# Optimization experiments

Hardware: AMD Instinct MI355X
Metric: run time of the kernel (lower is better)

## Reference

```python
import jax, jax.numpy as jnp
import numpy as np

# Static multi-level feature-map geometry (h, w) per level.
SPATIAL_SHAPES = np.array([[92, 92], [46, 46], [23, 23], [12, 12]], dtype=np.int32)
_AREAS = SPATIAL_SHAPES[:, 0] * SPATIAL_SHAPES[:, 1]
LEVEL_START = np.concatenate([[0], np.cumsum(_AREAS)[:-1]]).astype(np.int32)
LEN_IN = int(_AREAS.sum())  # 11253
N_HEADS, N_LEVELS, N_POINTS = 8, 4, 4
D_MODEL, D_HEAD = 256, 64


def setup_inputs() -> dict:
    key = jax.random.key(0)
    ks = jax.random.split(key, 12)
    N, Lq = 4, 1000
    s = 0.02
    f32 = jnp.float32
    return {
        'query': jax.random.normal(ks[0], (N, Lq, D_MODEL), f32),
        'reference_points': jax.random.uniform(ks[1], (N, Lq, N_LEVELS, 2), f32),
        'input_flatten': jax.random.normal(ks[2], (N, LEN_IN, D_MODEL), f32),
        'input_spatial_shapes': jnp.asarray(SPATIAL_SHAPES),
        'input_level_start_index': jnp.asarray(LEVEL_START),
        'W_off': jax.random.normal(ks[3], (N_HEADS * N_LEVELS * N_POINTS * 2, D_MODEL), f32) * s,
        'b_off': jax.random.normal(ks[4], (N_HEADS * N_LEVELS * N_POINTS * 2,), f32) * 0.5,
        'W_attn': jax.random.normal(ks[5], (N_HEADS * N_LEVELS * N_POINTS, D_MODEL), f32) * s,
        'b_attn': jax.random.normal(ks[6], (N_HEADS * N_LEVELS * N_POINTS,), f32) * s,
        'W_val': jax.random.normal(ks[7], (N_HEADS * D_HEAD, D_MODEL), f32) * s,
        'b_val': jnp.zeros((N_HEADS * D_HEAD,), f32),
        'W_out': jax.random.normal(ks[8], (D_MODEL, N_HEADS * D_HEAD), f32) * s,
        'b_out': jnp.zeros((D_MODEL,), f32),
    }


def _ms_deform_attn(value, sampling_locations, attention_weights):
    # value: [N, Len_in, H, D]; locations: [N, Lq, H, L, P, 2] in [0,1];
    # weights: [N, Lq, H, L, P] -> out [N, Lq, H*D]
    N, _, H, D = value.shape
    Lq, L, P = sampling_locations.shape[1], sampling_locations.shape[3], sampling_locations.shape[4]
    out = jnp.zeros((N, H, Lq, D), value.dtype)
    for l in range(L):
        h, w = int(SPATIAL_SHAPES[l, 0]), int(SPATIAL_SHAPES[l, 1])
        st = int(LEVEL_START[l])
        # per-level value as [N*H, h*w, D]
        v = value[:, st:st + h * w].transpose(0, 2, 1, 3).reshape(N * H, h * w, D)
        loc = sampling_locations[:, :, :, l].transpose(0, 2, 1, 3, 4).reshape(N * H, Lq * P, 2)
        aw = attention_weights[:, :, :, l].transpose(0, 2, 1, 3).reshape(N * H, Lq * P)
        # grid_sample align_corners=False convention (matches CUDA kernel)
        x = loc[..., 0] * w - 0.5
        y = loc[..., 1] * h - 0.5
        x0 = jnp.floor(x)
        y0 = jnp.floor(y)
        lx, ly = x - x0, y - y0
        x0i = x0.astype(jnp.int32)
        y0i = y0.astype(jnp.int32)

        def gather(yi, xi):
            valid = ((xi >= 0) & (xi < w) & (yi >= 0) & (yi < h)).astype(v.dtype)
            idx = jnp.clip(yi, 0, h - 1) * w + jnp.clip(xi, 0, w - 1)
            g = jnp.take_along_axis(v, idx[..., None], axis=1)  # [N*H, Lq*P, D]
            return g * valid[..., None]

        sampled = (gather(y0i, x0i) * ((1 - lx) * (1 - ly))[..., None]
                   + gather(y0i, x0i + 1) * (lx * (1 - ly))[..., None]
                   + gather(y0i + 1, x0i) * ((1 - lx) * ly)[..., None]
                   + gather(y0i + 1, x0i + 1) * (lx * ly)[..., None])
        out = out + (sampled * aw[..., None]).reshape(N, H, Lq, P, D).sum(axis=3)
    return out.transpose(0, 2, 1, 3).reshape(N, Lq, H * D)


def reference(query, reference_points, input_flatten, input_spatial_shapes,
              input_level_start_index, W_off, b_off, W_attn, b_attn,
              W_val, b_val, W_out, b_out):
    N, Lq, _ = query.shape
    Lin = input_flatten.shape[1]
    H, L, P, D = N_HEADS, N_LEVELS, N_POINTS, D_HEAD
    value = (input_flatten @ W_val.T + b_val).reshape(N, Lin, H, D)
    off = (query @ W_off.T + b_off).reshape(N, Lq, H, L, P, 2)
    aw = jax.nn.softmax((query @ W_attn.T + b_attn).reshape(N, Lq, H, L * P), axis=-1)
    aw = aw.reshape(N, Lq, H, L, P)
    # offset normalizer is (w, h) per level
    norm = jnp.asarray(SPATIAL_SHAPES[:, ::-1].copy(), jnp.float32)  # [L, 2]
    loc = reference_points[:, :, None, :, None, :] + off / norm[None, None, None, :, None, :]
    out = _ms_deform_attn(value, loc, aw)
    return out @ W_out.T + b_out
```

## Files before the change

### kernel.cpp

```cpp
#include <hip/hip_runtime.h>


typedef __attribute__((ext_vector_type(4))) float f32x4;
typedef __attribute__((ext_vector_type(8))) short bf16x8;
typedef __attribute__((ext_vector_type(4))) short bf16x4;

static __device__ __forceinline__ unsigned short f2bf(float f) {
    unsigned u = __builtin_bit_cast(unsigned, f);
    u += 0x7FFFu + ((u >> 16) & 1u);
    return (unsigned short)(u >> 16);
}
static __device__ __forceinline__ float bflo(unsigned d) {
    return __builtin_bit_cast(float, d << 16);
}
static __device__ __forceinline__ float bfhi(unsigned d) {
    return __builtin_bit_cast(float, d & 0xffff0000u);
}
static __device__ __forceinline__ void gload_lds16(const void* g, void* l) {
    __builtin_amdgcn_global_load_lds(
        (const __attribute__((address_space(1))) void*)g,
        (__attribute__((address_space(3))) void*)l, 16, 0, 0);
}

__global__ __launch_bounds__(256)
void cvt_k(const float* __restrict__ s0, const float* __restrict__ s1,
           const float* __restrict__ s2, const float* __restrict__ s3,
           const float* __restrict__ s4, const float* __restrict__ s5,
           unsigned short* __restrict__ dst) {
    const size_t i8 = ((size_t)blockIdx.x * 256 + threadIdx.x) * 8;
    if (i8 >= 12907520u) return;
    const float* sp; size_t loc;
    if (i8 < 11523072u)      { sp = s0; loc = i8; }
    else if (i8 < 12547072u) { sp = s1; loc = i8 - 11523072u; }
    else if (i8 < 12612608u) { sp = s2; loc = i8 - 12547072u; }
    else if (i8 < 12645376u) { sp = s3; loc = i8 - 12612608u; }
    else if (i8 < 12776448u) { sp = s4; loc = i8 - 12645376u; }
    else                     { sp = s5; loc = i8 - 12776448u; }
    f32x4 a = *(const f32x4*)(sp + loc);
    f32x4 b = *(const f32x4*)(sp + loc + 4);
    bf16x8 r;
    r[0] = f2bf(a[0]); r[1] = f2bf(a[1]); r[2] = f2bf(a[2]); r[3] = f2bf(a[3]);
    r[4] = f2bf(b[0]); r[5] = f2bf(b[1]); r[6] = f2bf(b[2]); r[7] = f2bf(b[3]);
    *(bf16x8*)(dst + i8) = r;
}

template<int MODE>
__global__ __launch_bounds__(256)
void gemm_bf16_tn(const unsigned short* __restrict__ A,
                  const unsigned short* __restrict__ B,
                  const float* __restrict__ bias, const float* __restrict__ bias2,
                  void* __restrict__ Cv, int M, int N, int K) {
    __shared__ __align__(16) char smem[65536];

    const int tid = threadIdx.x, lane = tid & 63, w = tid >> 6;
    const int wm = w >> 1, wn = w & 1;
    int bm, bn;
    if (MODE == 1) {
        const int bid = blockIdx.x;
        const int xcd = bid & 7;
        const int j   = bid >> 3;
        bm = xcd * 44 + (j >> 2);
        bn = j & 3;
    } else {
        bm = blockIdx.x; bn = blockIdx.y;
    }

    const int r8 = lane >> 3;
    const int colsrc = (((lane & 7) ^ r8) << 4);
    const char* pa[4]; const char* pb[4];
#pragma unroll
    for (int j = 0; j < 4; j++) {
        int ra = bm * 128 + j * 32 + w * 8 + r8; ra = ra < M ? ra : M - 1;
        int rb = bn * 128 + j * 32 + w * 8 + r8; rb = rb < N ? rb : N - 1;
        pa[j] = (const char*)A + (size_t)ra * ((size_t)K * 2) + colsrc;
        pb[j] = (const char*)B + (size_t)rb * ((size_t)K * 2) + colsrc;
    }
    const int ldso = w << 10;
    const int NT = K >> 6;

    f32x4 acc[4][4] = {};
    const int fr = lane & 15, fq = lane >> 4;
    const int k8b = fq << 4;
    const int swzR = (fr & 7) << 4;

#pragma unroll
    for (int j = 0; j < 4; j++) {
        gload_lds16(pa[j], smem + j * 4096 + ldso);
        gload_lds16(pb[j], smem + 16384 + j * 4096 + ldso);
    }
    __syncthreads();

    for (int t = 0; t < NT; ++t) {
        const int cur = (t & 1) << 15;
        if (t + 1 < NT) {
            const int nxt = ((t + 1) & 1) << 15;
            const int off = (t + 1) << 7;
#pragma unroll
            for (int j = 0; j < 4; j++) {
                gload_lds16(pa[j] + off, smem + nxt + j * 4096 + ldso);
                gload_lds16(pb[j] + off, smem + nxt + 16384 + j * 4096 + ldso);
            }
        }
#pragma unroll
        for (int kk = 0; kk < 2; ++kk) {
            const int ko = ((kk << 6) + k8b) ^ swzR;
            bf16x8 af[4], bv[4];
#pragma unroll
            for (int m = 0; m < 4; m++)
                af[m] = *(const bf16x8*)(smem + cur + ((wm * 64 + m * 16 + fr) << 7) + ko);
#pragma unroll
            for (int nn = 0; nn < 4; nn++)
                bv[nn] = *(const bf16x8*)(smem + cur + 16384 + ((wn * 64 + nn * 16 + fr) << 7) + ko);
#pragma unroll
            for (int m = 0; m < 4; m++)
#pragma unroll
                for (int nn = 0; nn < 4; nn++)
                    acc[m][nn] = __builtin_amdgcn_mfma_f32_16x16x32_bf16(
                        af[m], bv[nn], acc[m][nn], 0, 0, 0);
        }
        __syncthreads();
    }

    if (MODE != 1) {
        float* C = (float*)Cv;
        const int crow0 = bm * 128 + wm * 64 + fq * 4;
        const int ccol0 = bn * 128 + wn * 64 + fr;
#pragma unroll
        for (int m = 0; m < 4; m++) {
#pragma unroll
            for (int nn = 0; nn < 4; nn++) {
                const int col = ccol0 + nn * 16;
                const float bv2 = (MODE == 2 && col >= 256) ? bias2[col - 256]
                                                            : bias[col];
#pragma unroll
                for (int j = 0; j < 4; j++) {
                    const int row = crow0 + m * 16 + j;
                    if (row < M) C[(size_t)row * N + col] = acc[m][nn][j] + bv2;
                }
            }
        }
    } else {
        unsigned short* tile = (unsigned short*)smem + (size_t)w * (64 * 68);
        const int hh = bn * 2 + wn;
        float bvs[4];
#pragma unroll
        for (int nn = 0; nn < 4; nn++) bvs[nn] = bias[hh * 64 + nn * 16 + fr];
#pragma unroll
        for (int m = 0; m < 4; m++)
#pragma unroll
            for (int nn = 0; nn < 4; nn++)
#pragma unroll
                for (int j = 0; j < 4; j++)
                    tile[(m * 16 + fq * 4 + j) * 68 + nn * 16 + fr] =
                        f2bf(acc[m][nn][j] + bvs[nn]);
        __syncthreads();
        unsigned short* VT = (unsigned short*)Cv;
        const int q4 = (lane & 15) * 4;
        const int prow = lane >> 4;
#pragma unroll
        for (int it = 0; it < 16; ++it) {
            const int pl = it * 4 + prow;
            const int pixg = bm * 128 + wm * 64 + pl;
            if (pixg < M) {
                const int n = pixg / 11253;
                const int pix = pixg - n * 11253;
                bf16x4 v = *(const bf16x4*)&tile[pl * 68 + q4];
                *(bf16x4*)(VT + ((size_t)(n * 8 + hh) * 11253 + pix) * 64 + q4) = v;
            }
        }
    }
}

__global__ __launch_bounds__(256)
void sample_k(const unsigned short* __restrict__ valueT,
              const float* __restrict__ refp,
              const float* __restrict__ fused,
              unsigned int* __restrict__ msout)
{
    const int bid = blockIdx.x;
    const int xcd = bid & 7;
    const int jj  = bid >> 3;
    const int sl  = jj / 250;
    const int qb  = jj - sl * 250;
    const int nh  = xcd * 4 + sl;
    const int q   = __builtin_amdgcn_readfirstlane(qb * 4 + (threadIdx.x >> 6));
    const int lane = threadIdx.x & 63;
    const int g    = lane >> 5;
    const int n = nh >> 3, h = nh & 7;
    const int nq = n * 1000 + q;

    const float* lgp = fused + (size_t)nq * 384 + 256 + h * 16;
    float mx = lgp[0];
#pragma unroll
    for (int pp = 1; pp < 16; pp++) mx = fmaxf(mx, lgp[pp]);
    float s = 0.f;
#pragma unroll
    for (int pp = 0; pp < 16; pp++) s += __expf(lgp[pp] - mx);

    const int p  = lane & 15;
    const int lv = p >> 2;
    const int W  = lv == 0 ? 92 : lv == 1 ? 46 : lv == 2 ? 23 : 12;
    const int st = lv == 0 ? 0 : lv == 1 ? 8464 : lv == 2 ? 10580 : 11109;

    const float a  = __expf(lgp[p] - mx) / s;
    const float rx = refp[(size_t)nq * 8 + lv * 2 + 0];
    const float ry = refp[(size_t)nq * 8 + lv * 2 + 1];
    const float ox = fused[(size_t)nq * 384 + h * 32 + p * 2 + 0];
    const float oy = fused[(size_t)nq * 384 + h * 32 + p * 2 + 1];

    const float x = rx * (float)W + ox - 0.5f;
    const float y = ry * (float)W + oy - 0.5f;
    const float xf = floorf(x), yf = floorf(y);
    const int x0 = (int)xf, y0 = (int)yf;
    const float lx = x - xf, ly = y - yf;
    const int xb = min(max(x0, 0), W - 2);
    const int yb = min(max(y0, 0), W - 2);
    const float wx0 = (xb     == x0) ? (1.f - lx) : ((xb     == x0 + 1) ? lx : 0.f);
    const float wx1 = (xb + 1 == x0) ? (1.f - lx) : ((xb + 1 == x0 + 1) ? lx : 0.f);
    const float wy0 = (yb     == y0) ? (1.f - ly) : ((yb     == y0 + 1) ? ly : 0.f);
    const float wy1 = (yb + 1 == y0) ? (1.f - ly) : ((yb + 1 == y0 + 1) ? ly : 0.f);
    const int idx0v = st + yb * W + xb;
    const int idx1v = idx0v + W;
    const float wxs = (lane & 16) ? wx1 : wx0;
    const float wav = a * wxs * wy0;
    const float wbv = a * wxs * wy1;

    const unsigned int* vb =
        (const unsigned int*)valueT + (size_t)nh * 11253 * 32;

    float acc0 = 0.f, acc1 = 0.f;
    const int srcb = g << 4;
#pragma unroll
    for (int pp = 0; pp < 16; pp++) {
        const int src = pp + srcb;
        const int   i0 = __shfl(idx0v, src);
        const int   i1 = __shfl(idx1v, src);
        const float w0 = __shfl(wav,   src);
        const float w1 = __shfl(wbv,   src);
        const unsigned d0 = vb[i0 * 32 + lane];
        const unsigned d1 = vb[i1 * 32 + lane];
        acc0 = fmaf(w0, bflo(d0), acc0);
        acc1 = fmaf(w0, bfhi(d0), acc1);
        acc0 = fmaf(w1, bflo(d1), acc0);
        acc1 = fmaf(w1, bfhi(d1), acc1);
    }

    acc0 += __shfl(acc0, lane ^ 32);
    acc1 += __shfl(acc1, lane ^ 32);
    if (lane < 32) {
        const unsigned u = (unsigned)f2bf(acc0) | ((unsigned)f2bf(acc1) << 16);
        msout[(size_t)nq * 256 + h * 32 + (lane & 31)] = u;
    }
}

extern "C" void kernel_launch(void* const* d_in, const int* in_sizes, int n_in,
                              void* d_out, int out_size, void* d_ws, size_t ws_size,
                              hipStream_t stream) {
    (void)in_sizes; (void)n_in; (void)out_size; (void)ws_size;

    const float* query  = (const float*)d_in[0];
    const float* refp   = (const float*)d_in[1];
    const float* inpf   = (const float*)d_in[2];
    const float* W_off  = (const float*)d_in[5];
    const float* b_off  = (const float*)d_in[6];
    const float* W_attn = (const float*)d_in[7];
    const float* b_attn = (const float*)d_in[8];
    const float* W_val  = (const float*)d_in[9];
    const float* b_val  = (const float*)d_in[10];
    const float* W_out  = (const float*)d_in[11];
    const float* b_out  = (const float*)d_in[12];
    float* out = (float*)d_out;

    char* ws = (char*)d_ws;
    unsigned short* bf = (unsigned short*)ws;
    unsigned short* inpfb   = bf;
    unsigned short* queryb  = bf + 11523072;
    unsigned short* W_offb  = bf + 12547072;
    unsigned short* W_valb  = bf + 12645376;
    unsigned short* W_outb  = bf + 12776448;
    unsigned short* valueT  = (unsigned short*)(ws + 25815040);
    float* fusedb = (float*)(ws + 71907328);
    unsigned int* msoutu = (unsigned int*)(ws + 78051328);
    unsigned short* msoutb = (unsigned short*)msoutu;

    cvt_k<<<6303, 256, 0, stream>>>(inpf, query, W_off, W_attn, W_val, W_out, bf);
    gemm_bf16_tn<1><<<1408, 256, 0, stream>>>(
        inpfb, W_valb, b_val, nullptr, valueT, 45012, 512, 256);
    gemm_bf16_tn<2><<<dim3(32, 3), 256, 0, stream>>>(
        queryb, W_offb, b_off, b_attn, fusedb, 4000, 384, 256);
    sample_k<<<8000, 256, 0, stream>>>(valueT, refp, fusedb, msoutu);
    gemm_bf16_tn<0><<<dim3(32, 2), 256, 0, stream>>>(
        msoutb, W_outb, b_out, nullptr, out, 4000, 256, 512);
}
```

Measured before the change: 93.59 us.

## Fuse fp32-to-bf16 conversion into GEMM loaders and drop separate convert kernel

Removes the standalone conversion kernel that turned inputs and weights into bf16 in workspace. The GEMMs now load fp32 tiles from global memory into registers, pack them to bf16 with v_cvt_pk_bf16_f32, and store them swizzled into LDS, with register prefetch of the next tile overlapping the MFMA loop. This drops one launch and a full read-write round trip of the converted input. In exchange the GEMMs read twice as many bytes and give up the direct global-to-LDS loads for fp32 operands, which adds VGPR pressure and conversion work inside the kernel.

Result: slower. 120.4 us (+28.6%).

```diff
diff --git a/kernel.cpp b/kernel.cpp
--- a/kernel.cpp
+++ b/kernel.cpp
@@ -2,6 +2,7 @@
 
 
 typedef __attribute__((ext_vector_type(4))) float f32x4;
+typedef __attribute__((ext_vector_type(4))) unsigned int u32x4;
 typedef __attribute__((ext_vector_type(8))) short bf16x8;
 typedef __attribute__((ext_vector_type(4))) short bf16x4;
 
@@ -16,40 +17,23 @@
 static __device__ __forceinline__ float bfhi(unsigned d) {
     return __builtin_bit_cast(float, d & 0xffff0000u);
 }
+static __device__ __forceinline__ unsigned cvtpk(float lo, float hi) {
+    unsigned r;
+    asm("v_cvt_pk_bf16_f32 %0, %1, %2" : "=v"(r) : "v"(lo), "v"(hi));
+    return r;
+}
 static __device__ __forceinline__ void gload_lds16(const void* g, void* l) {
     __builtin_amdgcn_global_load_lds(
         (const __attribute__((address_space(1))) void*)g,
         (__attribute__((address_space(3))) void*)l, 16, 0, 0);
 }
 
-__global__ __launch_bounds__(256)
-void cvt_k(const float* __restrict__ s0, const float* __restrict__ s1,
-           const float* __restrict__ s2, const float* __restrict__ s3,
-           const float* __restrict__ s4, const float* __restrict__ s5,
-           unsigned short* __restrict__ dst) {
-    const size_t i8 = ((size_t)blockIdx.x * 256 + threadIdx.x) * 8;
-    if (i8 >= 12907520u) return;
-    const float* sp; size_t loc;
-    if (i8 < 11523072u)      { sp = s0; loc = i8; }
-    else if (i8 < 12547072u) { sp = s1; loc = i8 - 11523072u; }
-    else if (i8 < 12612608u) { sp = s2; loc = i8 - 12547072u; }
-    else if (i8 < 12645376u) { sp = s3; loc = i8 - 12612608u; }
-    else if (i8 < 12776448u) { sp = s4; loc = i8 - 12645376u; }
-    else                     { sp = s5; loc = i8 - 12776448u; }
-    f32x4 a = *(const f32x4*)(sp + loc);
-    f32x4 b = *(const f32x4*)(sp + loc + 4);
-    bf16x8 r;
-    r[0] = f2bf(a[0]); r[1] = f2bf(a[1]); r[2] = f2bf(a[2]); r[3] = f2bf(a[3]);
-    r[4] = f2bf(b[0]); r[5] = f2bf(b[1]); r[6] = f2bf(b[2]); r[7] = f2bf(b[3]);
-    *(bf16x8*)(dst + i8) = r;
-}
-
 template<int MODE>
 __global__ __launch_bounds__(256)
-void gemm_bf16_tn(const unsigned short* __restrict__ A,
-                  const unsigned short* __restrict__ B,
-                  const float* __restrict__ bias, const float* __restrict__ bias2,
-                  void* __restrict__ Cv, int M, int N, int K) {
+void gemm_k(const void* __restrict__ Av, const void* __restrict__ Bv,
+            const void* __restrict__ B2v,
+            const float* __restrict__ bias, const float* __restrict__ bias2,
+            void* __restrict__ Cv, int M, int N, int K) {
     __shared__ __align__(16) char smem[65536];
 
     const int tid = threadIdx.x, lane = tid & 63, w = tid >> 6;
@@ -65,42 +49,95 @@
         bm = blockIdx.x; bn = blockIdx.y;
     }
 
-    const int r8 = lane >> 3;
-    const int colsrc = (((lane & 7) ^ r8) << 4);
-    const char* pa[4]; const char* pb[4];
-#pragma unroll
-    for (int j = 0; j < 4; j++) {
-        int ra = bm * 128 + j * 32 + w * 8 + r8; ra = ra < M ? ra : M - 1;
-        int rb = bn * 128 + j * 32 + w * 8 + r8; rb = rb < N ? rb : N - 1;
-        pa[j] = (const char*)A + (size_t)ra * ((size_t)K * 2) + colsrc;
-        pb[j] = (const char*)B + (size_t)rb * ((size_t)K * 2) + colsrc;
-    }
+    const int sr = tid >> 1;
+    const int sh = (tid & 1) << 2;
+    int lofs[4];
+#pragma unroll
+    for (int i = 0; i < 4; i++)
+        lofs[i] = sr * 128 + (((sh + i) ^ (sr & 7)) << 4);
+
+    const char* asrc = nullptr;
+    const char* pa[4];
+    if (MODE == 0) {
+        const int r8 = lane >> 3;
+        const int cs16 = (((lane & 7) ^ r8) << 4);
+#pragma unroll
+        for (int j2 = 0; j2 < 4; j2++) {
+            int ra = bm * 128 + j2 * 32 + w * 8 + r8; ra = ra < M ? ra : M - 1;
+            pa[j2] = (const char*)Av + (size_t)ra * ((size_t)K * 2) + cs16;
+        }
+    } else {
+        int ra = bm * 128 + sr; ra = ra < M ? ra : M - 1;
+        asrc = (const char*)Av + (size_t)ra * ((size_t)K * 4);
+    }
+    const char* bsrc;
+    {
+        int rb = bn * 128 + sr; rb = rb < N ? rb : N - 1;
+        if (MODE == 2 && rb >= 256)
+            bsrc = (const char*)B2v + (size_t)(rb - 256) * ((size_t)K * 4);
+        else
+            bsrc = (const char*)Bv + (size_t)rb * ((size_t)K * 4);
+    }
+
     const int ldso = w << 10;
     const int NT = K >> 6;
+
+    f32x4 ar[8], br[8];
+    auto loadA = [&](int t) {
+        if (MODE != 0) {
+            const char* s = asrc + t * 256;
+#pragma unroll
+            for (int i = 0; i < 4; i++) {
+                ar[2 * i]     = *(const f32x4*)(s + (sh + i) * 32);
+                ar[2 * i + 1] = *(const f32x4*)(s + (sh + i) * 32 + 16);
+            }
+        } else {
+            const int off = t << 7;
+#pragma unroll
+            for (int j2 = 0; j2 < 4; j2++)
+                gload_lds16(pa[j2] + off, smem + ((t & 1) << 15) + j2 * 4096 + ldso);
+        }
+    };
+    auto loadB = [&](int t) {
+        const char* s = bsrc + t * 256;
+#pragma unroll
+        for (int i = 0; i < 4; i++) {
+            br[2 * i]     = *(const f32x4*)(s + (sh + i) * 32);
+            br[2 * i + 1] = *(const f32x4*)(s + (sh + i) * 32 + 16);
+        }
+    };
+    auto writeA = [&](int t) {
+        if (MODE != 0) {
+            char* base = smem + ((t & 1) << 15);
+#pragma unroll
+            for (int i = 0; i < 4; i++) {
+                u32x4 v = { cvtpk(ar[2*i][0], ar[2*i][1]), cvtpk(ar[2*i][2], ar[2*i][3]),
+                            cvtpk(ar[2*i+1][0], ar[2*i+1][1]), cvtpk(ar[2*i+1][2], ar[2*i+1][3]) };
+                *(u32x4*)(base + lofs[i]) = v;
+            }
+        }
+    };
+    auto writeB = [&](int t) {
+        char* base = smem + ((t & 1) << 15) + 16384;
+#pragma unroll
+        for (int i = 0; i < 4; i++) {
+            u32x4 v = { cvtpk(br[2*i][0], br[2*i][1]), cvtpk(br[2*i][2], br[2*i][3]),
+                        cvtpk(br[2*i+1][0], br[2*i+1][1]), cvtpk(br[2*i+1][2], br[2*i+1][3]) };
+            *(u32x4*)(base + lofs[i]) = v;
+        }
+    };
+
+    loadA(0); loadB(0); writeA(0); writeB(0);
+    __syncthreads();
 
     f32x4 acc[4][4] = {};
     const int fr = lane & 15, fq = lane >> 4;
     const int k8b = fq << 4;
     const int swzR = (fr & 7) << 4;
 
-#pragma unroll
-    for (int j = 0; j < 4; j++) {
-        gload_lds16(pa[j], smem + j * 4096 + ldso);
-        gload_lds16(pb[j], smem + 16384 + j * 4096 + ldso);
-    }
-    __syncthreads();
-
     for (int t = 0; t < NT; ++t) {
         const int cur = (t & 1) << 15;
-        if (t + 1 < NT) {
-            const int nxt = ((t + 1) & 1) << 15;
-            const int off = (t + 1) << 7;
-#pragma unroll
-            for (int j = 0; j < 4; j++) {
-                gload_lds16(pa[j] + off, smem + nxt + j * 4096 + ldso);
-                gload_lds16(pb[j] + off, smem + nxt + 16384 + j * 4096 + ldso);
-            }
-        }
+        if (t + 1 < NT) { loadA(t + 1); loadB(t + 1); }
 #pragma unroll
         for (int kk = 0; kk < 2; ++kk) {
             const int ko = ((kk << 6) + k8b) ^ swzR;
@@ -118,6 +155,7 @@
                     acc[m][nn] = __builtin_amdgcn_mfma_f32_16x16x32_bf16(
                         af[m], bv[nn], acc[m][nn], 0, 0, 0);
         }
+        if (t + 1 < NT) { writeA(t + 1); writeB(t + 1); }
         __syncthreads();
     }
 
@@ -272,23 +310,16 @@
     float* out = (float*)d_out;
 
     char* ws = (char*)d_ws;
-    unsigned short* bf = (unsigned short*)ws;
-    unsigned short* inpfb   = bf;
-    unsigned short* queryb  = bf + 11523072;
-    unsigned short* W_offb  = bf + 12547072;
-    unsigned short* W_valb  = bf + 12645376;
-    unsigned short* W_outb  = bf + 12776448;
-    unsigned short* valueT  = (unsigned short*)(ws + 25815040);
-    float* fusedb = (float*)(ws + 71907328);
-    unsigned int* msoutu = (unsigned int*)(ws + 78051328);
+    unsigned short* valueT = (unsigned short*)ws;
+    float* fusedb = (float*)(ws + 46092288);
+    unsigned int* msoutu = (unsigned int*)(ws + 52236288);
     unsigned short* msoutb = (unsigned short*)msoutu;
 
-    cvt_k<<<6303, 256, 0, stream>>>(inpf, query, W_off, W_attn, W_val, W_out, bf);
-    gemm_bf16_tn<1><<<1408, 256, 0, stream>>>(
-        inpfb, W_valb, b_val, nullptr, valueT, 45012, 512, 256);
-    gemm_bf16_tn<2><<<dim3(32, 3), 256, 0, stream>>>(
-        queryb, W_offb, b_off, b_attn, fusedb, 4000, 384, 256);
+    gemm_k<1><<<1408, 256, 0, stream>>>(
+        inpf, W_val, nullptr, b_val, nullptr, valueT, 45012, 512, 256);
+    gemm_k<2><<<dim3(32, 3), 256, 0, stream>>>(
+        query, W_off, W_attn, b_off, b_attn, fusedb, 4000, 384, 256);
     sample_k<<<8000, 256, 0, stream>>>(valueT, refp, fusedb, msoutu);
-    gemm_bf16_tn<0><<<dim3(32, 2), 256, 0, stream>>>(
-        msoutb, W_outb, b_out, nullptr, out, 4000, 256, 512);
-}
+    gemm_k<0><<<dim3(32, 2), 256, 0, stream>>>(
+        msoutb, W_out, nullptr, b_out, nullptr, out, 4000, 256, 512);
+}
```
